# Kernel optimization log

Measured on AMD Instinct MI355X. Metric: run time of the kernel, lower is better.

The kernel has to match this reference:

```python
import jax, jax.numpy as jnp
import numpy as np

DIM = 512
HID = 128
OUT = 32
ORDER = 3
B, L = 4, 4096


def positional_encoding(seq_len, d):
    pos = jnp.arange(seq_len, dtype=jnp.float32)[:, None]
    div = jnp.exp(-jnp.log(jnp.float32(10000.0)) * jnp.arange(0, d, 2, dtype=jnp.float32) / d)
    ang = pos * div[None, :]  # [L, d/2]
    pe = jnp.zeros((seq_len, d), dtype=jnp.float32)
    pe = pe.at[:, 0::2].set(jnp.sin(ang))
    pe = pe.at[:, 1::2].set(jnp.cos(ang))
    return pe


def setup_inputs() -> dict:
    key = jax.random.key(0)
    ks = jax.random.split(key, 9)
    s = lambda fan_in: 1.0 / np.sqrt(fan_in)
    return {
        "u": jax.random.normal(ks[0], (B, L, DIM), dtype=jnp.float32),
        "pW": jax.random.uniform(ks[1], (DIM, DIM * (ORDER + 1)), jnp.float32, -s(DIM), s(DIM)),
        "pb": jax.random.uniform(ks[2], (DIM * (ORDER + 1),), jnp.float32, -s(DIM), s(DIM)),
        "cW": jax.random.uniform(ks[3], (DIM * (ORDER + 1), DIM * (ORDER + 1), 3), jnp.float32, -s(DIM * 4 * 3), s(DIM * 4 * 3)),
        "cb": jax.random.uniform(ks[4], (DIM * (ORDER + 1),), jnp.float32, -s(DIM * 4 * 3), s(DIM * 4 * 3)),
        "fW": jax.random.uniform(ks[5], (HID, ORDER * DIM), jnp.float32, -s(HID), s(HID)),
        "fb": jax.random.uniform(ks[6], (ORDER * DIM,), jnp.float32, -s(HID), s(HID)),
        "oW": jax.random.uniform(ks[7], (DIM, OUT), jnp.float32, -s(DIM), s(DIM)),
        "ob": jax.random.uniform(ks[8], (OUT,), jnp.float32, -s(DIM), s(DIM)),
    }


def _fft_conv(h_filter, v):
    # circular conv along seq dim: h_filter [L, D], v [B, L, D]
    Vf = jnp.fft.rfft(v, axis=1)
    Hf = jnp.fft.rfft(h_filter, axis=0)[None, :, :]
    return jnp.fft.irfft(Vf * Hf, n=v.shape[1], axis=1)


def reference(u, pW, pb, cW, cb, fW, fb, oW, ob):
    seq_len = u.shape[1]
    t = positional_encoding(seq_len, HID)  # [L, HID]
    # hann window, periodic=False
    n = jnp.arange(seq_len, dtype=jnp.float32)
    window = (0.5 * (1.0 - jnp.cos(2.0 * jnp.pi * n / (seq_len - 1))))[:, None]  # [L,1]

    hat_z = u @ pW + pb  # [B, L, 4*DIM]
    # conv1d over seq with kernel 3, padding 1, channels 4*DIM -> 4*DIM
    z = jax.lax.conv_general_dilated(
        hat_z.transpose(0, 2, 1), cW, window_strides=(1,), padding=[(1, 1)],
        dimension_numbers=("NCH", "OIH", "NCH"))
    z = (z + cb[None, :, None]).transpose(0, 2, 1)  # [B, L, 4*DIM]

    v = z[:, :, :DIM]
    projs = z[:, :, DIM:]  # [B, L, 3*DIM]

    hat_h = t @ fW + fb  # [L, 3*DIM]
    h = hat_h * window  # [L, 3*DIM]

    for k in range(ORDER):
        xn = projs[:, :, DIM * k:DIM * (k + 1)]
        hn = h[:, DIM * k:DIM * (k + 1)]
        v = xn * _fft_conv(hn, v)

    return v @ oW + ob  # [B, L, OUT]
```

## Files before the change

### kernel.cpp

```cpp
#include <hip/hip_runtime.h>

typedef __attribute__((ext_vector_type(8))) short short8;
typedef __attribute__((ext_vector_type(4))) float f32x4;
typedef __attribute__((ext_vector_type(4))) unsigned short ushort4v;
typedef unsigned short ushortT;

#define PADROWS 4098
#define PI_F 3.14159265358979323f
#define PHYS(i) ((i) ^ (((i) >> 4) & 15))

__device__ __forceinline__ ushortT f2bf(float f) {
  union { float f; unsigned int u; } v; v.f = f;
  unsigned int r = (v.u + 0x7FFFu + ((v.u >> 16) & 1u)) >> 16;
  return (ushortT)r;
}
__device__ __forceinline__ float bf2f(ushortT b) {
  union { unsigned int u; float f; } v; v.u = ((unsigned int)b) << 16;
  return v.f;
}

__device__ __forceinline__ void gl2lds16(const void* g, void* l) {
  __builtin_amdgcn_global_load_lds((const __attribute__((address_space(1))) void*)g,
                                   (__attribute__((address_space(3))) void*)l, 16, 0, 0);
}


__global__ void cast_flat(const float* __restrict__ in, ushortT* __restrict__ outb) {
  size_t idx = (size_t)blockIdx.x * 256 + threadIdx.x;
  f32x4 v = *(const f32x4*)(in + idx * 4);
  ushort4v r;
  r[0] = f2bf(v[0]); r[1] = f2bf(v[1]); r[2] = f2bf(v[2]); r[3] = f2bf(v[3]);
  *(ushort4v*)(outb + idx * 4) = r;
}

__global__ void convert_u_pad(const float* __restrict__ in, ushortT* __restrict__ up) {
  size_t idx = (size_t)blockIdx.x * 256 + threadIdx.x;
  f32x4 v = *(const f32x4*)(in + idx * 4);
  ushort4v r;
  r[0] = f2bf(v[0]); r[1] = f2bf(v[1]); r[2] = f2bf(v[2]); r[3] = f2bf(v[3]);
  size_t g = idx * 4;
  int col = (int)(g & 511);
  int l = (int)(g >> 9);
  int b = l >> 12;
  *(ushort4v*)(up + ((size_t)b * PADROWS + (l & 4095) + 1) * 512 + col) = r;
}

__global__ void zero_pad_u(ushortT* __restrict__ Upad) {
  int idx = blockIdx.x * 256 + threadIdx.x;
  int col = idx & 511;
  int r = (idx >> 9) & 1;
  int b = idx >> 10;
  Upad[((size_t)b * PADROWS + (r ? 4097 : 0)) * 512 + col] = 0;
}

__global__ void convert_cW(const float* __restrict__ cW, ushortT* __restrict__ Wt) {
  size_t idx = (size_t)blockIdx.x * 256 + threadIdx.x;
  const float* p = cW + idx * 3;
  Wt[idx]           = f2bf(p[0]);
  Wt[idx + 4194304] = f2bf(p[1]);
  Wt[idx + 8388608] = f2bf(p[2]);
}

__global__ void pbc_kernel(const float* __restrict__ cW, const float* __restrict__ pb,
                           const float* __restrict__ cb, float* __restrict__ biasC,
                           float* __restrict__ pbC0, float* __restrict__ pbC2) {
  int o = blockIdx.x;
  int tid = threadIdx.x;
  float s0 = 0.f, s1 = 0.f, s2 = 0.f;
  const float* base = cW + (size_t)o * 2048 * 3;
  for (int i = tid; i < 2048; i += 256) {
    float p = pb[i];
    s0 = fmaf(p, base[i * 3 + 0], s0);
    s1 = fmaf(p, base[i * 3 + 1], s1);
    s2 = fmaf(p, base[i * 3 + 2], s2);
  }
#pragma unroll
  for (int off = 32; off >= 1; off >>= 1) {
    s0 += __shfl_down(s0, off);
    s1 += __shfl_down(s1, off);
    s2 += __shfl_down(s2, off);
  }
  __shared__ float red[4][3];
  if ((tid & 63) == 0) { red[tid >> 6][0] = s0; red[tid >> 6][1] = s1; red[tid >> 6][2] = s2; }
  __syncthreads();
  if (tid == 0) {
    float a0 = red[0][0] + red[1][0] + red[2][0] + red[3][0];
    float a1 = red[0][1] + red[1][1] + red[2][1] + red[3][1];
    float a2 = red[0][2] + red[1][2] + red[2][2] + red[3][2];
    biasC[o] = cb[o] + a0 + a1 + a2;
    pbC0[o] = a0;
    pbC2[o] = a2;
  }
}

__global__ void pe_window(float* __restrict__ tT, float* __restrict__ window) {
  int idx = blockIdx.x * 256 + threadIdx.x;
  int l = idx & 4095, d2 = idx >> 12;
  float dv = expf(-9.210340371976184f * (float)(2 * d2) / 128.0f);
  float ang = (float)l * dv;
  tT[(size_t)(2 * d2) * 4096 + l] = sinf(ang);
  tT[(size_t)(2 * d2 + 1) * 4096 + l] = cosf(ang);
  if (d2 == 0)
    window[l] = 0.5f * (1.0f - cosf(6.283185307179586f * (float)l / 4095.0f));
}

__global__ void fill_wtab(float2* __restrict__ Wg) {
  int m = blockIdx.x * 256 + threadIdx.x;
  float sn, cs;
  sincosf(-2.0f * PI_F * (float)m / 2048.0f, &sn, &cs);
  Wg[m] = make_float2(cs, sn);
}


__launch_bounds__(256, 2)
__global__ void gemm_fold(const ushortT* __restrict__ Wt, const ushortT* __restrict__ pW_bf,
                          ushortT* __restrict__ cWf) {
  __shared__ alignas(16) ushortT As[128 * 64];
  __shared__ alignas(16) ushortT Bs[128 * 64];
  const int tid = threadIdx.x;
  const int lane = tid & 63, w = tid >> 6;
  const int wm = w >> 1, wn = w & 1;
  const int tm = blockIdx.x, tn = blockIdx.y, h = blockIdx.z;
  const ushortT* A = Wt + (size_t)h * 4194304;
  f32x4 acc[4][4] = {};
#pragma unroll 1
  for (int kt = 0; kt < 32; ++kt) {
    const int i0 = kt * 64;
#pragma unroll
    for (int i = 0; i < 4; ++i) {
      int ldsoff = (i * 4 + w) * 1024;
      int m = ((i * 4 + w) << 3) + (lane >> 3);
      int col = (lane & 7) * 8;
      gl2lds16(A + (size_t)(tm * 128 + m) * 2048 + i0 + col, (char*)As + ldsoff);
      gl2lds16(pW_bf + (size_t)(tn * 128 + m) * 2048 + i0 + col, (char*)Bs + ldsoff);
    }
    __syncthreads();
#pragma unroll
    for (int ks = 0; ks < 2; ++ks) {
      short8 av[4], bv[4];
#pragma unroll
      for (int mi = 0; mi < 4; ++mi) {
        int row = wm * 64 + mi * 16 + (lane & 15);
        av[mi] = *(const short8*)(As + row * 64 + (ks * 4 + (lane >> 4)) * 8);
      }
#pragma unroll
      for (int ni = 0; ni < 4; ++ni) {
        int row = wn * 64 + ni * 16 + (lane & 15);
        bv[ni] = *(const short8*)(Bs + row * 64 + (ks * 4 + (lane >> 4)) * 8);
      }
#pragma unroll
      for (int mi = 0; mi < 4; ++mi)
#pragma unroll
        for (int ni = 0; ni < 4; ++ni)
          acc[mi][ni] = __builtin_amdgcn_mfma_f32_16x16x32_bf16(av[mi], bv[ni], acc[mi][ni], 0, 0, 0);
    }
    __syncthreads();
  }
#pragma unroll
  for (int mi = 0; mi < 4; ++mi)
#pragma unroll
    for (int ni = 0; ni < 4; ++ni) {
      int jc = tn * 128 + wn * 64 + ni * 16 + (lane & 15);
#pragma unroll
      for (int j = 0; j < 4; ++j) {
        int o = tm * 128 + wm * 64 + mi * 16 + (lane >> 4) * 4 + j;
        cWf[((size_t)h * 2048 + o) * 512 + jc] = f2bf(acc[mi][ni][j]);
      }
    }
}


__launch_bounds__(512, 2)
__global__ void gemm_conv8(const ushortT* __restrict__ Upad, const ushortT* __restrict__ cWf,
                           const float* __restrict__ biasC, const float* __restrict__ pbC0,
                           const float* __restrict__ pbC2, float* __restrict__ vT,
                           ushortT* __restrict__ projsT) {
  __shared__ ushortT lds[2][2][16384];
  const int tid = threadIdx.x;
  const int lane = tid & 63, w = tid >> 6;
  const int wm = w >> 2, wn = w & 3;
  int raw = blockIdx.x;
  int wg  = (raw & 7) * 64 + (raw >> 3);
  const int o0 = (wg >> 6) << 8;
  const int nt = wg & 63;
  const int b  = nt >> 4;
  const int l0 = (nt & 15) << 8;

  f32x4 acc[8][4] = {};
  short8 xf[4][2];

  const int sm = tid >> 3;
  const int sw1 = ((tid & 7) ^ (sm & 7)) << 3;

  auto stageW = [&](int slot, int half, int t) {
    int q = (t * 21846) >> 16, h = t - 3 * q, j0 = q << 6;
    size_t grow = (size_t)(h * 2048 + o0 + half * 128 + sm);
    char* dst = (char*)&lds[slot][0][0] + half * 16384 + w * 1024;
    gl2lds16(cWf + grow * 512 + j0 + sw1, dst);
    gl2lds16(cWf + (grow + 64) * 512 + j0 + sw1, dst + 8192);
  };
  auto stageX = [&](int slot, int half, int t) {
    int q = (t * 21846) >> 16, h = t - 3 * q, j0 = q << 6;
    size_t grow = (size_t)b * PADROWS + l0 + h + half * 128 + sm;
    char* dst = (char*)&lds[slot][1][0] + half * 16384 + w * 1024;
    gl2lds16(Upad + grow * 512 + j0 + sw1, dst);
    gl2lds16(Upad + (grow + 64) * 512 + j0 + sw1, dst + 8192);
  };
  auto ldsW = [&](int slot, int mi, int ks) -> short8 {
    int row = wm * 128 + mi * 16 + (lane & 15);
    int ch = (ks * 4 + (lane >> 4)) ^ (row & 7);
    return *(const short8*)&lds[slot][0][row * 64 + ch * 8];
  };
  auto ldsX = [&](int slot, int ni, int ks) -> short8 {
    int row = wn * 64 + ni * 16 + (lane & 15);
    int ch = (ks * 4 + (lane >> 4)) ^ (row & 7);
    return *(const short8*)&lds[slot][1][row * 64 + ch * 8];
  };

  stageW(0, 0, 0); stageW(0, 1, 0);
  stageX(0, 0, 0); stageX(0, 1, 0);
  stageX(1, 0, 1); stageX(1, 1, 1);
  asm volatile("s_waitcnt vmcnt(0)" ::: "memory");
  __builtin_amdgcn_s_barrier();

#define PHASE(slot, q, STAGECODE, VMCODE)                                                                    \
  {                                                                                                          \
    short8 w0k0 = ldsW(slot, 2*(q), 0), w0k1 = ldsW(slot, 2*(q), 1);                                         \
    short8 w1k0 = ldsW(slot, 2*(q)+1, 0), w1k1 = ldsW(slot, 2*(q)+1, 1);                                     \
    if ((q) == 0) {                                                                                          \
      _Pragma("unroll")                                                                                      \
      for (int ni = 0; ni < 4; ++ni) {                                                                       \
        xf[ni][0] = ldsX(slot, ni, 0);                                                                       \
        xf[ni][1] = ldsX(slot, ni, 1);                                                                       \
      }                                                                                                      \
    }                                                                                                        \
    STAGECODE;                                                                                               \
    VMCODE;                                                                                                  \
    __builtin_amdgcn_s_barrier();                                                                            \
    asm volatile("s_waitcnt lgkmcnt(0)" ::: "memory");                                                       \
    __builtin_amdgcn_sched_barrier(0);                                                                       \
    __builtin_amdgcn_s_setprio(1);                                                                           \
    _Pragma("unroll")                                                                                        \
    for (int ni = 0; ni < 4; ++ni) {                                                                         \
      acc[2*(q)][ni]   = __builtin_amdgcn_mfma_f32_16x16x32_bf16(w0k0, xf[ni][0], acc[2*(q)][ni], 0, 0, 0);  \
      acc[2*(q)][ni]   = __builtin_amdgcn_mfma_f32_16x16x32_bf16(w0k1, xf[ni][1], acc[2*(q)][ni], 0, 0, 0);  \
      acc[2*(q)+1][ni] = __builtin_amdgcn_mfma_f32_16x16x32_bf16(w1k0, xf[ni][0], acc[2*(q)+1][ni], 0, 0, 0);\
      acc[2*(q)+1][ni] = __builtin_amdgcn_mfma_f32_16x16x32_bf16(w1k1, xf[ni][1], acc[2*(q)+1][ni], 0, 0, 0);\
    }                                                                                                        \
    __builtin_amdgcn_s_setprio(0);                                                                           \
    __builtin_amdgcn_s_barrier();                                                                            \
  }

#pragma unroll 1
  for (int it = 0; it < 11; ++it) {
    const int t0 = 2 * it;
    PHASE(0, 0, stageW(1, 0, t0 + 1), );
    PHASE(0, 1, stageW(1, 1, t0 + 1), );
    PHASE(0, 2, stageX(0, 0, t0 + 2), );
    PHASE(0, 3, stageX(0, 1, t0 + 2), asm volatile("s_waitcnt vmcnt(4)" ::: "memory"));
    PHASE(1, 0, stageW(0, 0, t0 + 2), );
    PHASE(1, 1, stageW(0, 1, t0 + 2), );
    PHASE(1, 2, stageX(1, 0, t0 + 3), );
    PHASE(1, 3, stageX(1, 1, t0 + 3), asm volatile("s_waitcnt vmcnt(4)" ::: "memory"));
  }
  PHASE(0, 0, stageW(1, 0, 23), );
  PHASE(0, 1, stageW(1, 1, 23), );
  PHASE(0, 2, , );
  PHASE(0, 3, , asm volatile("s_waitcnt vmcnt(0)" ::: "memory"));
  PHASE(1, 0, , );
  PHASE(1, 1, , );
  PHASE(1, 2, , );
  PHASE(1, 3, , );
#undef PHASE

  const int r4 = (lane >> 4) * 4;
  const int lbase = l0 + wn * 64 + (lane & 15);
  if (o0 < 512) {
#pragma unroll
    for (int mi = 0; mi < 8; ++mi)
#pragma unroll
      for (int ni = 0; ni < 4; ++ni) {
        int l = lbase + ni * 16;
#pragma unroll
        for (int j = 0; j < 4; ++j) {
          int o = o0 + wm * 128 + mi * 16 + r4 + j;
          float val = acc[mi][ni][j] + biasC[o];
          if (l == 0) val -= pbC0[o];
          if (l == 4095) val -= pbC2[o];
          vT[((size_t)b * 512 + o) * 4096 + l] = val;
        }
      }
  } else {
#pragma unroll
    for (int mi = 0; mi < 8; ++mi)
#pragma unroll
      for (int ni = 0; ni < 4; ++ni) {
        int l = lbase + ni * 16;
#pragma unroll
        for (int j = 0; j < 4; ++j) {
          int o = o0 + wm * 128 + mi * 16 + r4 + j;
          float val = acc[mi][ni][j] + biasC[o];
          if (l == 0) val -= pbC0[o];
          if (l == 4095) val -= pbC2[o];
          int oc = o - 512;
          projsT[((size_t)((oc >> 9) * 4 + b) * 512 + (oc & 511)) * 4096 + l] = f2bf(val);
        }
      }
  }
}


__launch_bounds__(256, 1)
__global__ void h_kernel(const float* __restrict__ tT, const float* __restrict__ fW,
                         const float* __restrict__ fb, const float* __restrict__ window,
                         float* __restrict__ hT) {
  __shared__ float tTs[128][64];
  __shared__ float fWs[128][128];
  const int l0 = blockIdx.x * 64;
  const int c0 = blockIdx.y * 128;
  const int tid = threadIdx.x;
  {
    int lq = (tid & 15) * 4;
    int dr = tid >> 4;
#pragma unroll
    for (int d = dr; d < 128; d += 16)
      *(f32x4*)(&tTs[d][lq]) = *(const f32x4*)(tT + (size_t)d * 4096 + l0 + lq);
  }
  {
    int cq = (tid & 31) * 4;
    int dr = tid >> 5;
#pragma unroll
    for (int d = dr; d < 128; d += 8)
      *(f32x4*)(&fWs[d][cq]) = *(const f32x4*)(fW + (size_t)d * 1536 + c0 + cq);
  }
  __syncthreads();
  const int lgrp = tid & 15;
  const int cg = tid >> 4;
  float acc[8][4] = {};
#pragma unroll 4
  for (int d = 0; d < 128; ++d) {
    f32x4 tv = *(const f32x4*)(&tTs[d][lgrp * 4]);
#pragma unroll
    for (int j = 0; j < 8; ++j) {
      float wv = fWs[d][cg + 16 * j];
      acc[j][0] = fmaf(tv[0], wv, acc[j][0]);
      acc[j][1] = fmaf(tv[1], wv, acc[j][1]);
      acc[j][2] = fmaf(tv[2], wv, acc[j][2]);
      acc[j][3] = fmaf(tv[3], wv, acc[j][3]);
    }
  }
  f32x4 wl = *(const f32x4*)(window + l0 + lgrp * 4);
#pragma unroll
  for (int j = 0; j < 8; ++j) {
    int ch = c0 + cg + 16 * j;
    float fbv = fb[ch];
    f32x4 r;
    r[0] = (acc[j][0] + fbv) * wl[0];
    r[1] = (acc[j][1] + fbv) * wl[1];
    r[2] = (acc[j][2] + fbv) * wl[2];
    r[3] = (acc[j][3] + fbv) * wl[3];
    *(f32x4*)(hT + (size_t)ch * 4096 + l0 + lgrp * 4) = r;
  }
}


__device__ __forceinline__ float2 cadd(float2 a, float2 b){ return make_float2(a.x+b.x, a.y+b.y); }
__device__ __forceinline__ float2 csub(float2 a, float2 b){ return make_float2(a.x-b.x, a.y-b.y); }
__device__ __forceinline__ float2 cmulp(float2 a, float2 b){
  return make_float2(a.x*b.x - a.y*b.y, a.x*b.y + a.y*b.x);
}
template<bool INV>
__device__ __forceinline__ float2 tw_mul(float2 a, float2 w) {
  return INV ? make_float2(fmaf(a.x, w.x,  a.y*w.y), fmaf(a.y, w.x, -a.x*w.y))
             : make_float2(fmaf(a.x, w.x, -a.y*w.y), fmaf(a.x, w.y,  a.y*w.x));
}
template<bool INV>
__device__ __forceinline__ float2 rot(float2 z) {
  return INV ? make_float2(-z.y, z.x) : make_float2(z.y, -z.x);
}

template<bool INV, int NS>
__device__ __forceinline__ void stage_r8(float2* X, const float2* Wl, int t) {
  const float C7 = 0.70710678118654752f;
  float2 v[8];
#pragma unroll
  for (int r = 0; r < 8; ++r) v[r] = X[PHYS(t + 256 * r)];
  if (NS > 1) {
    const int jm = (t & (NS - 1)) * (256 / NS);
#pragma unroll
    for (int r = 1; r < 8; ++r) v[r] = tw_mul<INV>(v[r], Wl[PHYS(r * jm)]);
  }
  float2 a0 = cadd(v[0], v[4]), a1 = csub(v[0], v[4]);
  float2 a2 = cadd(v[2], v[6]), a3 = rot<INV>(csub(v[2], v[6]));
  float2 E0 = cadd(a0, a2), E1 = cadd(a1, a3), E2 = csub(a0, a2), E3 = csub(a1, a3);
  float2 b0 = cadd(v[1], v[5]), b1 = csub(v[1], v[5]);
  float2 b2 = cadd(v[3], v[7]), b3 = rot<INV>(csub(v[3], v[7]));
  float2 O0 = cadd(b0, b2), O1 = cadd(b1, b3), O2 = csub(b0, b2), O3 = csub(b1, b3);
  const float2 w1 = INV ? make_float2(C7, C7)  : make_float2(C7, -C7);
  const float2 w3 = INV ? make_float2(-C7, C7) : make_float2(-C7, -C7);
  O1 = cmulp(O1, w1);
  O2 = rot<INV>(O2);
  O3 = cmulp(O3, w3);
  __syncthreads();
  const int base = (t / NS) * (8 * NS) + (t % NS);
  X[PHYS(base)]          = cadd(E0, O0);
  X[PHYS(base + NS)]     = cadd(E1, O1);
  X[PHYS(base + 2*NS)]   = cadd(E2, O2);
  X[PHYS(base + 3*NS)]   = cadd(E3, O3);
  X[PHYS(base + 4*NS)]   = csub(E0, O0);
  X[PHYS(base + 5*NS)]   = csub(E1, O1);
  X[PHYS(base + 6*NS)]   = csub(E2, O2);
  X[PHYS(base + 7*NS)]   = csub(E3, O3);
  __syncthreads();
}

template<bool INV>
__device__ __forceinline__ void stage_r4(float2* X, const float2* Wl, int t) {
#pragma unroll
  for (int jj = 0; jj < 2; ++jj) {
    const int j = t + jj * 256;
    float2 v0 = X[PHYS(j)], v1 = X[PHYS(j + 512)], v2 = X[PHYS(j + 1024)], v3 = X[PHYS(j + 1536)];
    v1 = tw_mul<INV>(v1, Wl[PHYS(j)]);
    v2 = tw_mul<INV>(v2, Wl[PHYS(2 * j)]);
    v3 = tw_mul<INV>(v3, Wl[PHYS(3 * j)]);
    float2 a0 = cadd(v0, v2), a1 = csub(v0, v2), a2 = cadd(v1, v3), a3 = rot<INV>(csub(v1, v3));
    X[PHYS(j)]        = cadd(a0, a2);
    X[PHYS(j + 512)]  = cadd(a1, a3);
    X[PHYS(j + 1024)] = csub(a0, a2);
    X[PHYS(j + 1536)] = csub(a1, a3);
  }
  __syncthreads();
}

template<bool INV>
__device__ __forceinline__ void fft2048r8(float2* X, const float2* Wl, int t) {
  stage_r8<INV, 1>(X, Wl, t);
  stage_r8<INV, 8>(X, Wl, t);
  stage_r8<INV, 64>(X, Wl, t);
  stage_r4<INV>(X, Wl, t);
}

__launch_bounds__(256, 2)
__global__ void fft_filter_r(const float* __restrict__ hT, const float2* __restrict__ Wg,
                             float4* __restrict__ ABp) {
  __shared__ float2 X[2048];
  __shared__ float2 Wl[2048];
  __shared__ float2 H[2049];
  const int ch = blockIdx.x;
  const int tid = threadIdx.x;
  const float* sig = hT + (size_t)ch * 4096;
  for (int m = tid; m < 2048; m += 256) {
    Wl[PHYS(m)] = Wg[m];
    X[PHYS(m)] = *(const float2*)(sig + 2 * m);
  }
  __syncthreads();
  fft2048r8<false>(X, Wl, tid);
  for (int kk = tid; kk < 1024; kk += 256) {
    if (kk == 0) {
      float2 z0 = X[PHYS(0)];
      H[0]    = make_float2(z0.x + z0.y, 0.f);
      H[2048] = make_float2(z0.x - z0.y, 0.f);
      float2 zq = X[PHYS(1024)];
      H[1024] = make_float2(zq.x, -zq.y);
    } else {
      float2 zk = X[PHYS(kk)], zm = X[PHYS(2048 - kk)];
      float2 E = make_float2(0.5f * (zk.x + zm.x), 0.5f * (zk.y - zm.y));
      float2 D = make_float2(0.5f * (zk.x - zm.x), 0.5f * (zk.y + zm.y));
      float2 O = make_float2(D.y, -D.x);
      float sn, cs;
      __sincosf(-PI_F * (float)kk * (1.0f / 2048.0f), &sn, &cs);
      float2 twO = make_float2(O.x * cs - O.y * sn, O.x * sn + O.y * cs);
      H[kk]        = make_float2(E.x + twO.x, E.y + twO.y);
      H[2048 - kk] = make_float2(E.x - twO.x, -(E.y - twO.y));
    }
  }
  __syncthreads();
  float4* ab = ABp + ((size_t)ch << 11);
  for (int kk = tid; kk < 1024; kk += 256) {
    if (kk == 0) {
      float2 h0 = H[0], hM = H[2048], hq = H[1024];
      ab[0] = make_float4(0.5f * (h0.x + hM.x), 0.f, 0.f, 0.5f * (h0.x - hM.x));
      ab[1] = make_float4(hq.x, -hq.y, 0.f, 0.f);
    } else {
      float2 hk = H[kk], hm = H[2048 - kk];
      float sn, cs;
      __sincosf(PI_F * (float)kk * (1.0f / 2048.0f), &sn, &cs);
      float oms = 0.5f * (1.f - sn), ops = 0.5f * (1.f + sn), ch2 = 0.5f * cs;
      float2 al1 = make_float2(oms * hk.x + ops * hm.x, oms * hk.y - ops * hm.y);
      float2 d1  = make_float2(hk.x - hm.x, hk.y + hm.y);
      float2 be1 = make_float2(-ch2 * d1.y, ch2 * d1.x);
      float2 al2 = make_float2(oms * hm.x + ops * hk.x, oms * hm.y - ops * hk.y);
      float2 d2  = make_float2(hm.x - hk.x, hm.y + hk.y);
      float2 be2 = make_float2(ch2 * d2.y, -ch2 * d2.x);
      ab[2 * kk]     = make_float4(al1.x, al1.y, be1.x, be1.y);
      ab[2 * kk + 1] = make_float4(al2.x, al2.y, be2.x, be2.y);
    }
  }
}

__launch_bounds__(256, 4)
__global__ void fft_conv3(float* __restrict__ vT, const ushortT* __restrict__ projsT,
                          const float4* __restrict__ ABp, const float2* __restrict__ Wg) {
  __shared__ float2 X[2048];
  __shared__ float2 Wl[2048];
  const int bc = blockIdx.x;
  const int c = bc & 511, b = bc >> 9;
  const int tid = threadIdx.x;
  float* sig = vT + (size_t)bc * 4096;
  for (int m = tid; m < 2048; m += 256) {
    Wl[PHYS(m)] = Wg[m];
    X[PHYS(m)] = *(const float2*)(sig + 2 * m);
  }
  __syncthreads();
  fft2048r8<false>(X, Wl, tid);
  const float scale = 1.0f / 2048.0f;
#pragma unroll 1
  for (int k = 0; k < 3; ++k) {
    const float4* ab = ABp + ((size_t)(k * 512 + c) << 11);
    for (int kk = tid; kk < 1024; kk += 256) {
      float4 A1 = ab[2 * kk], A2 = ab[2 * kk + 1];
      int e2 = kk ? 2048 - kk : 1024;
      float2 Zk = X[PHYS(kk)], Zm = X[PHYS(e2)];
      float2 c1 = kk ? Zm : Zk;
      float2 c2 = kk ? Zk : Zm;
      float2 Wk, Wm;
      Wk.x = A1.x * Zk.x - A1.y * Zk.y + A1.z * c1.x + A1.w * c1.y;
      Wk.y = A1.x * Zk.y + A1.y * Zk.x - A1.z * c1.y + A1.w * c1.x;
      Wm.x = A2.x * Zm.x - A2.y * Zm.y + A2.z * c2.x + A2.w * c2.y;
      Wm.y = A2.x * Zm.y + A2.y * Zm.x - A2.z * c2.y + A2.w * c2.x;
      X[PHYS(kk)] = Wk;
      X[PHYS(e2)] = Wm;
    }
    __syncthreads();
    fft2048r8<true>(X, Wl, tid);
    const ushortT* xn = projsT + ((size_t)(k * 4 + b) * 512 + c) * 4096;
    if (k < 2) {
      for (int m = tid; m < 2048; m += 256) {
        unsigned int pr = *(const unsigned int*)(xn + 2 * m);
        float2 a = X[PHYS(m)];
        X[PHYS(m)] = make_float2(a.x * scale * bf2f((ushortT)(pr & 0xffffu)),
                                 a.y * scale * bf2f((ushortT)(pr >> 16)));
      }
      __syncthreads();
      fft2048r8<false>(X, Wl, tid);
    } else {
      for (int m = tid; m < 2048; m += 256) {
        unsigned int pr = *(const unsigned int*)(xn + 2 * m);
        float2 a = X[PHYS(m)];
        *(float2*)(sig + 2 * m) = make_float2(a.x * scale * bf2f((ushortT)(pr & 0xffffu)),
                                              a.y * scale * bf2f((ushortT)(pr >> 16)));
      }
    }
  }
}


__launch_bounds__(256)
__global__ void out_gemm(const float* __restrict__ vT, const float* __restrict__ oW,
                         const float* __restrict__ ob, float* __restrict__ out) {
  int l0 = blockIdx.x * 32;
  int b = l0 >> 12;
  int li = threadIdx.x & 31;
  int og = (threadIdx.x >> 5) * 4;
  float acc[4] = {};
  const float* vb = vT + (size_t)b * 512 * 4096 + (l0 & 4095) + li;
#pragma unroll 8
  for (int c = 0; c < 512; ++c) {
    float v = vb[(size_t)c * 4096];
#pragma unroll
    for (int j = 0; j < 4; ++j)
      acc[j] = fmaf(v, oW[c * 32 + og + j], acc[j]);
  }
  float* op = out + (size_t)(l0 + li) * 32 + og;
  f32x4 r;
  r[0] = acc[0] + ob[og];     r[1] = acc[1] + ob[og + 1];
  r[2] = acc[2] + ob[og + 2]; r[3] = acc[3] + ob[og + 3];
  *(f32x4*)op = r;
}


__global__ void ws_sentinel(float* __restrict__ out) {
  if (threadIdx.x == 0) out[0] = -31337.0f;
}


extern "C" void kernel_launch(void* const* d_in, const int* in_sizes, int n_in,
                              void* d_out, int out_size, void* d_ws, size_t ws_size,
                              hipStream_t stream) {
  (void)in_sizes; (void)n_in; (void)out_size;
  const float* u  = (const float*)d_in[0];
  const float* pW = (const float*)d_in[1];
  const float* pb = (const float*)d_in[2];
  const float* cW = (const float*)d_in[3];
  const float* cb = (const float*)d_in[4];
  const float* fW = (const float*)d_in[5];
  const float* fb = (const float*)d_in[6];
  const float* oW = (const float*)d_in[7];
  const float* ob = (const float*)d_in[8];
  float* out = (float*)d_out;

  char* ws = (char*)d_ws;
  ushortT* Upad   = (ushortT*)(ws);
  ushortT* cWf    = (ushortT*)(ws + 16785408);
  float*   biasC  = (float*)  (ws + 23076864);
  float*   pbC0   = (float*)  (ws + 23085056);
  float*   pbC2   = (float*)  (ws + 23093248);
  float2*  Wg     = (float2*) (ws + 23101440);
  float4*  ABp    = (float4*) (ws + 23117824);
  float*   vT     = (float*)  (ws + 73449472);
  ushortT* projsT = (ushortT*)(ws + 107003904);
  const size_t total = 157335552;
  char* S = (char*)vT;
  ushortT* Wt     = (ushortT*)(S);
  ushortT* pW_bf  = (ushortT*)(S + 25165824);
  float*   tT     = (float*)  (S + 27262976);
  float*   window = (float*)  (S + 29360128);
  float*   hT     = (float*)  (S + 29376512);

  if (total > ws_size) {
    ws_sentinel<<<1, 64, 0, stream>>>(out);
    return;
  }

  convert_u_pad<<<8192, 256, 0, stream>>>(u, Upad);
  zero_pad_u<<<16, 256, 0, stream>>>(Upad);
  cast_flat<<<1024, 256, 0, stream>>>(pW, pW_bf);
  convert_cW<<<16384, 256, 0, stream>>>(cW, Wt);
  pbc_kernel<<<2048, 256, 0, stream>>>(cW, pb, cb, biasC, pbC0, pbC2);
  gemm_fold<<<dim3(16, 4, 3), 256, 0, stream>>>(Wt, pW_bf, cWf);
  pe_window<<<1024, 256, 0, stream>>>(tT, window);
  fill_wtab<<<8, 256, 0, stream>>>(Wg);
  h_kernel<<<dim3(64, 12), 256, 0, stream>>>(tT, fW, fb, window, hT);
  fft_filter_r<<<1536, 256, 0, stream>>>(hT, Wg, ABp);
  gemm_conv8<<<512, 512, 0, stream>>>(Upad, cWf, biasC, pbC0, pbC2, vT, projsT);
  fft_conv3<<<2048, 256, 0, stream>>>(vT, projsT, ABp, Wg);
  out_gemm<<<512, 256, 0, stream>>>(vT, oW, ob, out);
}
```

Measured before the change: 352.8 us.

## Fuse setup kernels, store raw filter spectrum, and tile output GEMM via LDS

Merges the pad zeroing into the u conversion, the cW bf16 cast into the bias-fold reduction, and computes positional encoding and window inline in h_kernel instead of separate kernels. The filter FFT now stores the plain half spectrum (float2, half the size of the old alpha/beta float4 table), and fft_conv3 rebuilds the alpha/beta coefficients on the fly using a precomputed sin/cos table in LDS, trading extra ALU for less global traffic. The output GEMM is restructured to stage vT and oW tiles in shared memory with 8 outputs per thread. Fewer launches and less memory traffic are the aim, at the cost of more per-element arithmetic in the conv kernel.

```diff
diff --git a/kernel.cpp b/kernel.cpp
--- a/kernel.cpp
+++ b/kernel.cpp
@@ -6,6 +6,7 @@
 typedef unsigned short ushortT;
 
 #define PADROWS 4098
+#define HSTR 2056
 #define PI_F 3.14159265358979323f
 #define PHYS(i) ((i) ^ (((i) >> 4) & 15))
 
@@ -34,7 +35,16 @@
 }
 
 __global__ void convert_u_pad(const float* __restrict__ in, ushortT* __restrict__ up) {
-  size_t idx = (size_t)blockIdx.x * 256 + threadIdx.x;
+  int blk = blockIdx.x;
+  if (blk >= 8192) {
+    int idx = (blk - 8192) * 256 + threadIdx.x;
+    int col = idx & 511;
+    int r = (idx >> 9) & 1;
+    int b = idx >> 10;
+    up[((size_t)b * PADROWS + (r ? 4097 : 0)) * 512 + col] = 0;
+    return;
+  }
+  size_t idx = (size_t)blk * 256 + threadIdx.x;
   f32x4 v = *(const f32x4*)(in + idx * 4);
   ushort4v r;
   r[0] = f2bf(v[0]); r[1] = f2bf(v[1]); r[2] = f2bf(v[2]); r[3] = f2bf(v[3]);
@@ -45,34 +55,24 @@
   *(ushort4v*)(up + ((size_t)b * PADROWS + (l & 4095) + 1) * 512 + col) = r;
 }
 
-__global__ void zero_pad_u(ushortT* __restrict__ Upad) {
-  int idx = blockIdx.x * 256 + threadIdx.x;
-  int col = idx & 511;
-  int r = (idx >> 9) & 1;
-  int b = idx >> 10;
-  Upad[((size_t)b * PADROWS + (r ? 4097 : 0)) * 512 + col] = 0;
-}
-
-__global__ void convert_cW(const float* __restrict__ cW, ushortT* __restrict__ Wt) {
-  size_t idx = (size_t)blockIdx.x * 256 + threadIdx.x;
-  const float* p = cW + idx * 3;
-  Wt[idx]           = f2bf(p[0]);
-  Wt[idx + 4194304] = f2bf(p[1]);
-  Wt[idx + 8388608] = f2bf(p[2]);
-}
-
-__global__ void pbc_kernel(const float* __restrict__ cW, const float* __restrict__ pb,
-                           const float* __restrict__ cb, float* __restrict__ biasC,
-                           float* __restrict__ pbC0, float* __restrict__ pbC2) {
+__global__ void cwt_pbc(const float* __restrict__ cW, const float* __restrict__ pb,
+                        const float* __restrict__ cb, ushortT* __restrict__ Wt,
+                        float* __restrict__ biasC, float* __restrict__ pbC0,
+                        float* __restrict__ pbC2) {
   int o = blockIdx.x;
   int tid = threadIdx.x;
   float s0 = 0.f, s1 = 0.f, s2 = 0.f;
-  const float* base = cW + (size_t)o * 2048 * 3;
+  const float* base = cW + (size_t)o * 6144;
   for (int i = tid; i < 2048; i += 256) {
+    float w0 = base[i * 3], w1 = base[i * 3 + 1], w2 = base[i * 3 + 2];
+    size_t oi = (size_t)o * 2048 + i;
+    Wt[oi]           = f2bf(w0);
+    Wt[oi + 4194304] = f2bf(w1);
+    Wt[oi + 8388608] = f2bf(w2);
     float p = pb[i];
-    s0 = fmaf(p, base[i * 3 + 0], s0);
-    s1 = fmaf(p, base[i * 3 + 1], s1);
-    s2 = fmaf(p, base[i * 3 + 2], s2);
+    s0 = fmaf(p, w0, s0);
+    s1 = fmaf(p, w1, s1);
+    s2 = fmaf(p, w2, s2);
   }
 #pragma unroll
   for (int off = 32; off >= 1; off >>= 1) {
@@ -93,22 +93,17 @@
   }
 }
 
-__global__ void pe_window(float* __restrict__ tT, float* __restrict__ window) {
-  int idx = blockIdx.x * 256 + threadIdx.x;
-  int l = idx & 4095, d2 = idx >> 12;
-  float dv = expf(-9.210340371976184f * (float)(2 * d2) / 128.0f);
-  float ang = (float)l * dv;
-  tT[(size_t)(2 * d2) * 4096 + l] = sinf(ang);
-  tT[(size_t)(2 * d2 + 1) * 4096 + l] = cosf(ang);
-  if (d2 == 0)
-    window[l] = 0.5f * (1.0f - cosf(6.283185307179586f * (float)l / 4095.0f));
-}
-
-__global__ void fill_wtab(float2* __restrict__ Wg) {
+__global__ void fill_tabs(float2* __restrict__ Wg, float2* __restrict__ Sg) {
   int m = blockIdx.x * 256 + threadIdx.x;
   float sn, cs;
-  sincosf(-2.0f * PI_F * (float)m / 2048.0f, &sn, &cs);
-  Wg[m] = make_float2(cs, sn);
+  if (m < 2048) {
+    sincosf(-2.0f * PI_F * (float)m / 2048.0f, &sn, &cs);
+    Wg[m] = make_float2(cs, sn);
+  } else {
+    int k = m - 2048;
+    sincosf(PI_F * (float)k / 2048.0f, &sn, &cs);
+    Sg[k] = make_float2(cs, sn);
+  }
 }
 
 
@@ -311,20 +306,19 @@
 
 
 __launch_bounds__(256, 1)
-__global__ void h_kernel(const float* __restrict__ tT, const float* __restrict__ fW,
-                         const float* __restrict__ fb, const float* __restrict__ window,
+__global__ void h_kernel(const float* __restrict__ fW, const float* __restrict__ fb,
                          float* __restrict__ hT) {
   __shared__ float tTs[128][64];
   __shared__ float fWs[128][128];
   const int l0 = blockIdx.x * 64;
   const int c0 = blockIdx.y * 128;
   const int tid = threadIdx.x;
-  {
-    int lq = (tid & 15) * 4;
-    int dr = tid >> 4;
-#pragma unroll
-    for (int d = dr; d < 128; d += 16)
-      *(f32x4*)(&tTs[d][lq]) = *(const f32x4*)(tT + (size_t)d * 4096 + l0 + lq);
+  for (int r = tid; r < 4096; r += 256) {
+    int d2 = r >> 6, li = r & 63;
+    float dv = expf(-9.210340371976184f * (float)(2 * d2) / 128.0f);
+    float ang = (float)(l0 + li) * dv;
+    tTs[2 * d2][li] = sinf(ang);
+    tTs[2 * d2 + 1][li] = cosf(ang);
   }
   {
     int cq = (tid & 31) * 4;
@@ -349,7 +343,12 @@
       acc[j][3] = fmaf(tv[3], wv, acc[j][3]);
     }
   }
-  f32x4 wl = *(const f32x4*)(window + l0 + lgrp * 4);
+  f32x4 wl;
+#pragma unroll
+  for (int j = 0; j < 4; ++j) {
+    int l = l0 + lgrp * 4 + j;
+    wl[j] = 0.5f * (1.0f - cosf(6.283185307179586f * (float)l / 4095.0f));
+  }
 #pragma unroll
   for (int j = 0; j < 8; ++j) {
     int ch = c0 + cg + 16 * j;
@@ -440,12 +439,11 @@
   stage_r4<INV>(X, Wl, t);
 }
 
-__launch_bounds__(256, 2)
+__launch_bounds__(256, 4)
 __global__ void fft_filter_r(const float* __restrict__ hT, const float2* __restrict__ Wg,
-                             float4* __restrict__ ABp) {
+                             float2* __restrict__ Hf) {
   __shared__ float2 X[2048];
   __shared__ float2 Wl[2048];
-  __shared__ float2 H[2049];
   const int ch = blockIdx.x;
   const int tid = threadIdx.x;
   const float* sig = hT + (size_t)ch * 4096;
@@ -455,13 +453,14 @@
   }
   __syncthreads();
   fft2048r8<false>(X, Wl, tid);
+  float2* o = Hf + (size_t)ch * HSTR;
   for (int kk = tid; kk < 1024; kk += 256) {
     if (kk == 0) {
       float2 z0 = X[PHYS(0)];
-      H[0]    = make_float2(z0.x + z0.y, 0.f);
-      H[2048] = make_float2(z0.x - z0.y, 0.f);
+      o[0]    = make_float2(z0.x + z0.y, 0.f);
+      o[2048] = make_float2(z0.x - z0.y, 0.f);
       float2 zq = X[PHYS(1024)];
-      H[1024] = make_float2(zq.x, -zq.y);
+      o[1024] = make_float2(zq.x, -zq.y);
     } else {
       float2 zk = X[PHYS(kk)], zm = X[PHYS(2048 - kk)];
       float2 E = make_float2(0.5f * (zk.x + zm.x), 0.5f * (zk.y - zm.y));
@@ -470,39 +469,19 @@
       float sn, cs;
       __sincosf(-PI_F * (float)kk * (1.0f / 2048.0f), &sn, &cs);
       float2 twO = make_float2(O.x * cs - O.y * sn, O.x * sn + O.y * cs);
-      H[kk]        = make_float2(E.x + twO.x, E.y + twO.y);
-      H[2048 - kk] = make_float2(E.x - twO.x, -(E.y - twO.y));
-    }
-  }
-  __syncthreads();
-  float4* ab = ABp + ((size_t)ch << 11);
-  for (int kk = tid; kk < 1024; kk += 256) {
-    if (kk == 0) {
-      float2 h0 = H[0], hM = H[2048], hq = H[1024];
-      ab[0] = make_float4(0.5f * (h0.x + hM.x), 0.f, 0.f, 0.5f * (h0.x - hM.x));
-      ab[1] = make_float4(hq.x, -hq.y, 0.f, 0.f);
-    } else {
-      float2 hk = H[kk], hm = H[2048 - kk];
-      float sn, cs;
-      __sincosf(PI_F * (float)kk * (1.0f / 2048.0f), &sn, &cs);
-      float oms = 0.5f * (1.f - sn), ops = 0.5f * (1.f + sn), ch2 = 0.5f * cs;
-      float2 al1 = make_float2(oms * hk.x + ops * hm.x, oms * hk.y - ops * hm.y);
-      float2 d1  = make_float2(hk.x - hm.x, hk.y + hm.y);
-      float2 be1 = make_float2(-ch2 * d1.y, ch2 * d1.x);
-      float2 al2 = make_float2(oms * hm.x + ops * hk.x, oms * hm.y - ops * hk.y);
-      float2 d2  = make_float2(hm.x - hk.x, hm.y + hk.y);
-      float2 be2 = make_float2(ch2 * d2.y, -ch2 * d2.x);
-      ab[2 * kk]     = make_float4(al1.x, al1.y, be1.x, be1.y);
-      ab[2 * kk + 1] = make_float4(al2.x, al2.y, be2.x, be2.y);
+      o[kk]        = make_float2(E.x + twO.x, E.y + twO.y);
+      o[2048 - kk] = make_float2(E.x - twO.x, -(E.y - twO.y));
     }
   }
 }
 
 __launch_bounds__(256, 4)
 __global__ void fft_conv3(float* __restrict__ vT, const ushortT* __restrict__ projsT,
-                          const float4* __restrict__ ABp, const float2* __restrict__ Wg) {
+                          const float2* __restrict__ Hf, const float2* __restrict__ Wg,
+                          const float2* __restrict__ Sg) {
   __shared__ float2 X[2048];
   __shared__ float2 Wl[2048];
+  __shared__ float2 S[1024];
   const int bc = blockIdx.x;
   const int c = bc & 511, b = bc >> 9;
   const int tid = threadIdx.x;
@@ -511,25 +490,36 @@
     Wl[PHYS(m)] = Wg[m];
     X[PHYS(m)] = *(const float2*)(sig + 2 * m);
   }
+  for (int m = tid; m < 1024; m += 256) S[m] = Sg[m];
   __syncthreads();
   fft2048r8<false>(X, Wl, tid);
   const float scale = 1.0f / 2048.0f;
 #pragma unroll 1
   for (int k = 0; k < 3; ++k) {
-    const float4* ab = ABp + ((size_t)(k * 512 + c) << 11);
+    const float2* H = Hf + (size_t)(k * 512 + c) * HSTR;
     for (int kk = tid; kk < 1024; kk += 256) {
-      float4 A1 = ab[2 * kk], A2 = ab[2 * kk + 1];
-      int e2 = kk ? 2048 - kk : 1024;
-      float2 Zk = X[PHYS(kk)], Zm = X[PHYS(e2)];
-      float2 c1 = kk ? Zm : Zk;
-      float2 c2 = kk ? Zk : Zm;
-      float2 Wk, Wm;
-      Wk.x = A1.x * Zk.x - A1.y * Zk.y + A1.z * c1.x + A1.w * c1.y;
-      Wk.y = A1.x * Zk.y + A1.y * Zk.x - A1.z * c1.y + A1.w * c1.x;
-      Wm.x = A2.x * Zm.x - A2.y * Zm.y + A2.z * c2.x + A2.w * c2.y;
-      Wm.y = A2.x * Zm.y + A2.y * Zm.x - A2.z * c2.y + A2.w * c2.x;
-      X[PHYS(kk)] = Wk;
-      X[PHYS(e2)] = Wm;
+      if (kk == 0) {
+        float h0x = H[0].x, hMx = H[2048].x;
+        float2 hq = H[1024];
+        float a1r = 0.5f * (h0x + hMx), a1w = 0.5f * (h0x - hMx);
+        float2 Z0 = X[PHYS(0)], Zq = X[PHYS(1024)];
+        X[PHYS(0)]    = make_float2(a1r * Z0.x + a1w * Z0.y, a1r * Z0.y + a1w * Z0.x);
+        X[PHYS(1024)] = make_float2(hq.x * Zq.x + hq.y * Zq.y, hq.x * Zq.y - hq.y * Zq.x);
+      } else {
+        float2 hk = H[kk], hm = H[2048 - kk];
+        float cs = S[kk].x, sn = S[kk].y;
+        float oms = 0.5f * (1.f - sn), ops = 0.5f * (1.f + sn), c2h = 0.5f * cs;
+        float d1x = hk.x - hm.x, d1y = hk.y + hm.y;
+        float a1x = oms * hk.x + ops * hm.x, a1y = oms * hk.y - ops * hm.y;
+        float b1x = -c2h * d1y, b1y = c2h * d1x;
+        float a2x = oms * hm.x + ops * hk.x, a2y = oms * hm.y - ops * hk.y;
+        float b2x = c2h * d1y, b2y = c2h * d1x;
+        float2 Zk = X[PHYS(kk)], Zm = X[PHYS(2048 - kk)];
+        X[PHYS(kk)] = make_float2(a1x * Zk.x - a1y * Zk.y + b1x * Zm.x + b1y * Zm.y,
+                                  a1x * Zk.y + a1y * Zk.x - b1x * Zm.y + b1y * Zm.x);
+        X[PHYS(2048 - kk)] = make_float2(a2x * Zm.x - a2y * Zm.y + b2x * Zk.x + b2y * Zk.y,
+                                         a2x * Zm.y + a2y * Zm.x - b2x * Zk.y + b2y * Zk.x);
+      }
     }
     __syncthreads();
     fft2048r8<true>(X, Wl, tid);
@@ -555,27 +545,46 @@
 }
 
 
-__launch_bounds__(256)
+__launch_bounds__(256, 2)
 __global__ void out_gemm(const float* __restrict__ vT, const float* __restrict__ oW,
                          const float* __restrict__ ob, float* __restrict__ out) {
-  int l0 = blockIdx.x * 32;
-  int b = l0 >> 12;
-  int li = threadIdx.x & 31;
-  int og = (threadIdx.x >> 5) * 4;
-  float acc[4] = {};
-  const float* vb = vT + (size_t)b * 512 * 4096 + (l0 & 4095) + li;
+  __shared__ float vs[64][68];
+  __shared__ float ows[64][36];
+  const int l0 = blockIdx.x * 64;
+  const int b = l0 >> 12;
+  const int tid = threadIdx.x;
+  const int l = tid & 63;
+  const int og = (tid >> 6) * 8;
+  float acc[8] = {};
+  const float* vb = vT + (size_t)b * 2097152 + (l0 & 4095);
+  const int cs = tid >> 2;
+  const int lq = (tid & 3) * 16;
+  const int oq = (tid & 3) * 8;
+#pragma unroll 1
+  for (int cc = 0; cc < 512; cc += 64) {
+#pragma unroll
+    for (int i = 0; i < 4; ++i)
+      *(f32x4*)(&vs[cs][lq + i * 4]) = *(const f32x4*)(vb + (size_t)(cc + cs) * 4096 + lq + i * 4);
+    *(f32x4*)(&ows[cs][oq])     = *(const f32x4*)(oW + (cc + cs) * 32 + oq);
+    *(f32x4*)(&ows[cs][oq + 4]) = *(const f32x4*)(oW + (cc + cs) * 32 + oq + 4);
+    __syncthreads();
 #pragma unroll 8
-  for (int c = 0; c < 512; ++c) {
-    float v = vb[(size_t)c * 4096];
-#pragma unroll
-    for (int j = 0; j < 4; ++j)
-      acc[j] = fmaf(v, oW[c * 32 + og + j], acc[j]);
-  }
-  float* op = out + (size_t)(l0 + li) * 32 + og;
-  f32x4 r;
-  r[0] = acc[0] + ob[og];     r[1] = acc[1] + ob[og + 1];
-  r[2] = acc[2] + ob[og + 2]; r[3] = acc[3] + ob[og + 3];
-  *(f32x4*)op = r;
+    for (int c3 = 0; c3 < 64; ++c3) {
+      float v = vs[c3][l];
+#pragma unroll
+      for (int j = 0; j < 8; ++j)
+        acc[j] = fmaf(v, ows[c3][og + j], acc[j]);
+    }
+    __syncthreads();
+  }
+  float* op = out + (size_t)(l0 + l) * 32 + og;
+  f32x4 r0, r1;
+  r0[0] = acc[0] + ob[og];     r0[1] = acc[1] + ob[og + 1];
+  r0[2] = acc[2] + ob[og + 2]; r0[3] = acc[3] + ob[og + 3];
+  r1[0] = acc[4] + ob[og + 4]; r1[1] = acc[5] + ob[og + 5];
+  r1[2] = acc[6] + ob[og + 6]; r1[3] = acc[7] + ob[og + 7];
+  *(f32x4*)op = r0;
+  *(f32x4*)(op + 4) = r1;
 }
 
 
@@ -606,33 +615,29 @@
   float*   pbC0   = (float*)  (ws + 23085056);
   float*   pbC2   = (float*)  (ws + 23093248);
   float2*  Wg     = (float2*) (ws + 23101440);
-  float4*  ABp    = (float4*) (ws + 23117824);
-  float*   vT     = (float*)  (ws + 73449472);
-  ushortT* projsT = (ushortT*)(ws + 107003904);
-  const size_t total = 157335552;
+  float2*  Sg     = (float2*) (ws + 23117824);
+  float2*  Hf     = (float2*) (ws + 23126016);
+  float*   vT     = (float*)  (ws + 48390144);
+  ushortT* projsT = (ushortT*)(ws + 81944576);
+  const size_t total = 132276224;
   char* S = (char*)vT;
   ushortT* Wt     = (ushortT*)(S);
   ushortT* pW_bf  = (ushortT*)(S + 25165824);
-  float*   tT     = (float*)  (S + 27262976);
-  float*   window = (float*)  (S + 29360128);
-  float*   hT     = (float*)  (S + 29376512);
+  float*   hT     = (float*)  (S + 27262976);
 
   if (total > ws_size) {
     ws_sentinel<<<1, 64, 0, stream>>>(out);
     return;
   }
 
-  convert_u_pad<<<8192, 256, 0, stream>>>(u, Upad);
-  zero_pad_u<<<16, 256, 0, stream>>>(Upad);
+  convert_u_pad<<<8208, 256, 0, stream>>>(u, Upad);
   cast_flat<<<1024, 256, 0, stream>>>(pW, pW_bf);
-  convert_cW<<<16384, 256, 0, stream>>>(cW, Wt);
-  pbc_kernel<<<2048, 256, 0, stream>>>(cW, pb, cb, biasC, pbC0, pbC2);
+  cwt_pbc<<<2048, 256, 0, stream>>>(cW, pb, cb, Wt, biasC, pbC0, pbC2);
+  fill_tabs<<<12, 256, 0, stream>>>(Wg, Sg);
   gemm_fold<<<dim3(16, 4, 3), 256, 0, stream>>>(Wt, pW_bf, cWf);
-  pe_window<<<1024, 256, 0, stream>>>(tT, window);
-  fill_wtab<<<8, 256, 0, stream>>>(Wg);
-  h_kernel<<<dim3(64, 12), 256, 0, stream>>>(tT, fW, fb, window, hT);
-  fft_filter_r<<<1536, 256, 0, stream>>>(hT, Wg, ABp);
+  h_kernel<<<dim3(64, 12), 256, 0, stream>>>(fW, fb, hT);
+  fft_filter_r<<<1536, 256, 0, stream>>>(hT, Wg, Hf);
   gemm_conv8<<<512, 512, 0, stream>>>(Upad, cWf, biasC, pbC0, pbC2, vT, projsT);
-  fft_conv3<<<2048, 256, 0, stream>>>(vT, projsT, ABp, Wg);
-  out_gemm<<<512, 256, 0, stream>>>(vT, oW, ob, out);
-}
+  fft_conv3<<<2048, 256, 0, stream>>>(vT, projsT, Hf, Wg, Sg);
+  out_gemm<<<256, 256, 0, stream>>>(vT, oW, ob, out);
+}
```

New measurement: 318.8 us. -9.6%, faster.
